# Kernel optimization log

Measured on AMD Instinct MI355X. Metric: run time of the kernel, lower is better.

## Reference

```python
import jax, jax.numpy as jnp
import numpy as np
from jax import lax

B, CIN, T = 16, 2, 4096
DM, DI, DS, DR, DC, NL = 128, 256, 16, 8, 4, 6  # d_model, d_inner, d_state, dt_rank, d_conv, n_layers


def setup_inputs():
    ks = iter(jax.random.split(jax.random.key(0), 48))
    def rn(shape, s=0.05):
        return jax.random.normal(next(ks), shape, jnp.float32) * s
    rng = np.random.default_rng(0)
    n_mask = int(round(0.25 / 0.02))
    starts = rng.choice(np.linspace(0.0, 1.0, int(round(1 / 0.02)), endpoint=False), n_mask, replace=False)
    m = np.ones((B, CIN, T), np.float32)
    for s0 in starts:
        m[:, :, int(T * s0):int(T * (s0 + 0.02))] = 0.0
    return {
        'x': jax.random.normal(next(ks), (B, CIN, T), jnp.float32),
        'mask': jnp.asarray(m),
        'enc_W0': rn((32, CIN, 3), 0.3), 'enc_b0': jnp.zeros(32), 'enc_g0': jnp.ones(32), 'enc_be0': jnp.zeros(32),
        'enc_W1': rn((64, 32, 3), 0.1), 'enc_b1': jnp.zeros(64), 'enc_g1': jnp.ones(64), 'enc_be1': jnp.zeros(64),
        'enc_W2': rn((128, 64, 3), 0.08), 'enc_b2': jnp.zeros(128), 'enc_g2': jnp.ones(128), 'enc_be2': jnp.zeros(128),
        'ln_g': jnp.ones((NL, DM)), 'ln_b': jnp.zeros((NL, DM)),
        'in_W': rn((NL, 2 * DI, DM)), 'conv_W': rn((NL, DI, DC), 0.3), 'conv_b': jnp.zeros((NL, DI)),
        'xp_W': rn((NL, DR + 2 * DS, DI)), 'dt_W': rn((NL, DI, DR), 0.2),
        'dt_b': jnp.full((NL, DI), -4.6, jnp.float32),  # softplus -> dt ~ 0.01
        'A_log': jnp.tile(jnp.log(jnp.arange(1, DS + 1, dtype=jnp.float32)), (NL, DI, 1)),
        'D_p': jnp.ones((NL, DI)), 'out_W': rn((NL, DM, DI)),
        'nf_g': jnp.ones(DM), 'nf_b': jnp.zeros(DM),
        'dec_W0': rn((128, 64, 3), 0.08), 'dec_b0': jnp.zeros(64), 'dec_g0': jnp.ones(64), 'dec_be0': jnp.zeros(64),
        'dec_W1': rn((64, 32, 3), 0.1), 'dec_b1': jnp.zeros(32), 'dec_g1': jnp.ones(32), 'dec_be1': jnp.zeros(32),
        'dec_W2': rn((32, CIN, 3), 0.1), 'dec_b2': jnp.zeros(CIN),
    }


def _conv(x, W, b, stride, pad):
    y = lax.conv_general_dilated(x, W, (stride,), [(pad, pad)], dimension_numbers=('NCH', 'OIH', 'NCH'))
    return y + b[None, :, None]


def _deconv(x, W, b, stride=2, pad=1, out_pad=1):
    # torch ConvTranspose1d weight (in, out, k) -> flipped conv with lhs dilation
    k = W.shape[-1]
    Wc = jnp.flip(W, -1).transpose(1, 0, 2)
    y = lax.conv_general_dilated(x, Wc, (1,), [(k - 1 - pad, k - 1 - pad + out_pad)],
                                 lhs_dilation=(stride,), dimension_numbers=('NCH', 'OIH', 'NCH'))
    return y + b[None, :, None]


def _gn1(x, g, b, eps=1e-5):  # GroupNorm(1, C) over (C, L)
    m = x.mean((1, 2), keepdims=True)
    v = ((x - m) ** 2).mean((1, 2), keepdims=True)
    return (x - m) * lax.rsqrt(v + eps) * g[None, :, None] + b[None, :, None]


def _ln(x, g, b, eps=1e-5):
    m = x.mean(-1, keepdims=True)
    v = ((x - m) ** 2).mean(-1, keepdims=True)
    return (x - m) * lax.rsqrt(v + eps) * g + b


def _mamba(u, in_W, conv_W, conv_b, xp_W, dt_W, dt_b, A_log, D_p, out_W):
    # u: (B, L, DM)
    xz = jnp.einsum('bld,ed->ble', u, in_W)            # (B, L, 2*DI)
    xi, z = xz[..., :DI], xz[..., DI:]
    xc = jnp.pad(xi.transpose(0, 2, 1), ((0, 0), (0, 0), (DC - 1, 0)))  # causal pad
    xc = lax.conv_general_dilated(xc, conv_W[:, None, :], (1,), [(0, 0)],
                                  feature_group_count=DI, dimension_numbers=('NCH', 'OIH', 'NCH'))
    xc = jax.nn.silu(xc + conv_b[None, :, None]).transpose(0, 2, 1)     # (B, L, DI)
    dbl = jnp.einsum('bld,ed->ble', xc, xp_W)          # (B, L, DR+2*DS)
    dt = jax.nn.softplus(jnp.einsum('blr,dr->bld', dbl[..., :DR], dt_W) + dt_b)
    Bm = dbl[..., DR:DR + DS]
    Cm = dbl[..., DR + DS:]
    A = -jnp.exp(A_log)                                # (DI, DS)
    dA = jnp.exp(dt[..., None] * A)                    # (B, L, DI, DS)
    dBx = dt[..., None] * Bm[:, :, None, :] * xc[..., None]
    def comb(e1, e2):
        a1, b1 = e1
        a2, b2 = e2
        return a1 * a2, a2 * b1 + b2
    _, h = lax.associative_scan(comb, (dA, dBx), axis=1)  # selective scan over L
    y = jnp.einsum('blds,bls->bld', h, Cm) + D_p * xc
    y = y * jax.nn.silu(z)
    return jnp.einsum('bld,ed->ble', y, out_W)          # (B, L, DM)


def _forward(x, mask, enc_W0, enc_b0, enc_g0, enc_be0, enc_W1, enc_b1, enc_g1, enc_be1,
             enc_W2, enc_b2, enc_g2, enc_be2, ln_g, ln_b, in_W, conv_W, conv_b, xp_W,
             dt_W, dt_b, A_log, D_p, out_W, nf_g, nf_b,
             dec_W0, dec_b0, dec_g0, dec_be0, dec_W1, dec_b1, dec_g1, dec_be1, dec_W2, dec_b2):
    gelu = lambda t: jax.nn.gelu(t, approximate=False)
    h = mask * x
    h = gelu(_gn1(_conv(h, enc_W0, enc_b0, 2, 1), enc_g0, enc_be0))
    h = gelu(_gn1(_conv(h, enc_W1, enc_b1, 2, 1), enc_g1, enc_be1))
    h = gelu(_gn1(_conv(h, enc_W2, enc_b2, 2, 1), enc_g2, enc_be2))
    s = h.transpose(0, 2, 1)                            # (B, L=T/8, DM)
    for i in range(NL):
        s = s + _mamba(_ln(s, ln_g[i], ln_b[i]), in_W[i], conv_W[i], conv_b[i],
                       xp_W[i], dt_W[i], dt_b[i], A_log[i], D_p[i], out_W[i])
    s = _ln(s, nf_g, nf_b)
    d = s.transpose(0, 2, 1)
    d = gelu(_gn1(_deconv(d, dec_W0, dec_b0), dec_g0, dec_be0))
    d = gelu(_gn1(_deconv(d, dec_W1, dec_b1), dec_g1, dec_be1))
    d = _deconv(d, dec_W2, dec_b2)                      # (B, CIN, T), no norm/act on last block
    return d


def reference(x, mask, enc_W0, enc_b0, enc_g0, enc_be0, enc_W1, enc_b1, enc_g1, enc_be1,
              enc_W2, enc_b2, enc_g2, enc_be2, ln_g, ln_b, in_W, conv_W, conv_b, xp_W,
              dt_W, dt_b, A_log, D_p, out_W, nf_g, nf_b,
              dec_W0, dec_b0, dec_g0, dec_be0, dec_W1, dec_b1, dec_g1, dec_be1, dec_W2, dec_b2):
    d = _forward(x, mask, enc_W0, enc_b0, enc_g0, enc_be0, enc_W1, enc_b1, enc_g1, enc_be1,
                 enc_W2, enc_b2, enc_g2, enc_be2, ln_g, ln_b, in_W, conv_W, conv_b, xp_W,
                 dt_W, dt_b, A_log, D_p, out_W, nf_g, nf_b,
                 dec_W0, dec_b0, dec_g0, dec_be0, dec_W1, dec_b1, dec_g1, dec_be1, dec_W2, dec_b2)
    return (d, x, mask)
```

## Files before the change

kernel.cpp:

```cpp
#include <hip/hip_runtime.h>
#include <hip/hip_bf16.h>
#include <math.h>

#define NB 16
#define TT 4096
#define LL 512
#define DM 128
#define DI 256
#define NLAYER 6
#define CL 32
#define NCH 16

typedef __bf16 bf16x8 __attribute__((ext_vector_type(8)));
typedef float f32x4 __attribute__((ext_vector_type(4)));
typedef unsigned short ushort;

static __device__ __forceinline__ float gelu_f(float v){
  return 0.5f*v*(1.f + erff(v*0.70710678118654752f));
}
static __device__ __forceinline__ float silu_f(float v){
  return v/(1.f + __expf(-v));
}
static __device__ __forceinline__ ushort f2b(float v){
  __hip_bfloat16 h = __float2bfloat16(v);
  return *(ushort*)&h;
}

__global__ __launch_bounds__(256) void k_maskmul(const float* __restrict__ x, const float* __restrict__ m,
                          float* __restrict__ out, int n){
  int i = blockIdx.x*256 + threadIdx.x;
  if (i < n) out[i] = x[i]*m[i];
}

__global__ __launch_bounds__(256) void k_castb(const float* __restrict__ in, ushort* __restrict__ out, int n){
  int i = blockIdx.x*256 + threadIdx.x;
  if (i < n) out[i] = f2b(in[i]);
}

__global__ __launch_bounds__(256) void k_trw(const float* __restrict__ in, float* __restrict__ out, int Ci, int Co){
  int idx = blockIdx.x*256 + threadIdx.x;
  int n = Ci*Co*3;
  if (idx >= n) return;
  int k = idx % 3;
  int o = (idx/3) % Co;
  int ci = idx/(3*Co);
  out[((size_t)o*Ci + ci)*3 + k] = in[idx];
}

template<int Ci, int Co, int TW, int OS>
__global__ __launch_bounds__(256) void k_conv_lds(const float* __restrict__ x, const float* __restrict__ W,
                        const float* __restrict__ bias, float* __restrict__ y, int Li){
  const int Lc = TW;
  const int Lo = Li >> 1;
  const int S  = Lo / Lc;
  const int CoB = Co / OS;
  __shared__ float xe[Ci][Lc+1];
  __shared__ float xo[Ci][Lc+1];
  int bid = blockIdx.x;
  int os = bid % OS;
  int ch = (bid / OS) % S;
  int b  = bid / (OS*S);
  int t0 = ch*Lc;
  const float* xb = x + (size_t)b*Ci*Li;
  for (int idx = threadIdx.x; idx < Ci*(2*Lc+1); idx += 256){
    int ci = idx / (2*Lc+1);
    int j  = idx - ci*(2*Lc+1);
    int gin = 2*t0 - 1 + j;
    float v = (gin >= 0 && gin < Li) ? xb[(size_t)ci*Li + gin] : 0.f;
    if (j & 1) xo[ci][j>>1] = v;
    else       xe[ci][j>>1] = v;
  }
  __syncthreads();
  const int NOg = 256/TW;
  const int OI  = CoB/NOg;
  int tl = threadIdx.x % TW;
  int og = threadIdx.x / TW;
  #pragma unroll
  for (int oi = 0; oi < OI; oi++){
    int o = os*CoB + oi*NOg + og;
    const float* w = W + (size_t)o*Ci*3;
    float acc = bias[o];
    #pragma unroll 4
    for (int ci = 0; ci < Ci; ci++){
      float w0 = w[ci*3+0], w1 = w[ci*3+1], w2 = w[ci*3+2];
      acc += w0*xe[ci][tl] + w1*xo[ci][tl] + w2*xe[ci][tl+1];
    }
    y[((size_t)b*Co + o)*Lo + t0 + tl] = acc;
  }
}

__global__ __launch_bounds__(256) void k_gn_part(const float* __restrict__ x, float* __restrict__ gp){
  int b = blockIdx.x >> 3, k8 = blockIdx.x & 7;
  const float* xb = x + (size_t)b*65536 + (size_t)k8*8192;
  float s = 0.f, s2 = 0.f;
  for (int i = threadIdx.x; i < 8192; i += 256){ float v = xb[i]; s += v; s2 += v*v; }
  #pragma unroll
  for (int o = 32; o; o >>= 1){ s += __shfl_down(s, o); s2 += __shfl_down(s2, o); }
  __shared__ float sh[8];
  int wid = threadIdx.x >> 6;
  if ((threadIdx.x & 63) == 0){ sh[wid] = s; sh[wid+4] = s2; }
  __syncthreads();
  if (threadIdx.x == 0){
    float a = sh[0]+sh[1]+sh[2]+sh[3], a2 = sh[4]+sh[5]+sh[6]+sh[7];
    gp[(b*8+k8)*2+0] = a; gp[(b*8+k8)*2+1] = a2;
  }
}
__global__ __launch_bounds__(256) void k_gn_apply(float* __restrict__ x, const float* __restrict__ g,
                          const float* __restrict__ be, int Tl, const float* __restrict__ gp){
  int gidx = blockIdx.x*256 + threadIdx.x;
  int b = gidx >> 16, i = gidx & 65535;
  float s = 0.f, s2 = 0.f;
  #pragma unroll
  for (int k = 0; k < 8; k++){ s += gp[(b*8+k)*2]; s2 += gp[(b*8+k)*2+1]; }
  float mean = s*(1.f/65536.f);
  float inv  = rsqrtf(s2*(1.f/65536.f) - mean*mean + 1e-5f);
  int c = i / Tl;
  float* p = x + (size_t)b*65536 + i;
  float v = (*p - mean)*inv*g[c] + be[c];
  *p = gelu_f(v);
}

__global__ __launch_bounds__(256) void k_transpose2(const float* __restrict__ in, float* __restrict__ out){
  int idx = blockIdx.x*256 + threadIdx.x;
  if (idx >= NB*DM*LL) return;
  int t = idx & 511;
  int c = (idx >> 9) & 127;
  int b = idx >> 16;
  out[(size_t)b*65536 + (size_t)t*128 + c] = in[idx];
}

__global__ __launch_bounds__(256) void k_transposeB(const float* __restrict__ in, float* __restrict__ out){
  int idx = blockIdx.x*256 + threadIdx.x;
  if (idx >= NB*DM*LL) return;
  int m = idx & 511;
  int c = (idx >> 9) & 127;
  int b = idx >> 16;
  out[idx] = in[(size_t)b*65536 + (size_t)m*128 + c];
}

__global__ __launch_bounds__(256) void k_ln2(const float* __restrict__ x, const float* __restrict__ g,
                      const float* __restrict__ be, float* __restrict__ out, int rows){
  int row = blockIdx.x*4 + (threadIdx.x >> 6);
  if (row >= rows) return;
  int lid = threadIdx.x & 63;
  const float* xr = x + (size_t)row*DM;
  float v0 = xr[lid], v1 = xr[lid+64];
  float s = v0 + v1;
  #pragma unroll
  for (int o = 32; o; o >>= 1) s += __shfl_xor(s, o);
  float mean = s*(1.f/128.f);
  float d0 = v0-mean, d1 = v1-mean;
  float s2 = d0*d0 + d1*d1;
  #pragma unroll
  for (int o = 32; o; o >>= 1) s2 += __shfl_xor(s2, o);
  float inv = rsqrtf(s2*(1.f/128.f) + 1e-5f);
  float* orow = out + (size_t)row*DM;
  orow[lid]    = d0*inv*g[lid]    + be[lid];
  orow[lid+64] = d1*inv*g[lid+64] + be[lid+64];
}

__global__ __launch_bounds__(256) void k_ln2b(const float* __restrict__ x, const float* __restrict__ g,
                      const float* __restrict__ be, ushort* __restrict__ out, int rows){
  int row = blockIdx.x*4 + (threadIdx.x >> 6);
  if (row >= rows) return;
  int lid = threadIdx.x & 63;
  const float* xr = x + (size_t)row*DM;
  float v0 = xr[lid], v1 = xr[lid+64];
  float s = v0 + v1;
  #pragma unroll
  for (int o = 32; o; o >>= 1) s += __shfl_xor(s, o);
  float mean = s*(1.f/128.f);
  float d0 = v0-mean, d1 = v1-mean;
  float s2 = d0*d0 + d1*d1;
  #pragma unroll
  for (int o = 32; o; o >>= 1) s2 += __shfl_xor(s2, o);
  float inv = rsqrtf(s2*(1.f/128.f) + 1e-5f);
  ushort* orow = out + (size_t)row*DM;
  orow[lid]    = f2b(d0*inv*g[lid]    + be[lid]);
  orow[lid+64] = f2b(d1*inv*g[lid+64] + be[lid+64]);
}

__global__ __launch_bounds__(256) void k_mfma_split(const ushort* __restrict__ A, const ushort* __restrict__ B,
                          float* __restrict__ C0, float* __restrict__ C1, int K){
  int tid = threadIdx.x;
  int wid = tid >> 6, l = tid & 63;
  int wm = wid >> 1, wn = wid & 1;
  int m0 = blockIdx.y*128 + wm*64;
  int n0 = blockIdx.x*128 + wn*64;
  int lr = l & 15;
  int lk = (l >> 4)*8;
  int orow = (l >> 4)*4;
  f32x4 acc[4][4];
  #pragma unroll
  for (int i = 0; i < 4; i++)
    #pragma unroll
    for (int j = 0; j < 4; j++) acc[i][j] = (f32x4){0.f,0.f,0.f,0.f};
  for (int k0 = 0; k0 < K; k0 += 32){
    bf16x8 a[4], b[4];
    #pragma unroll
    for (int f = 0; f < 4; f++)
      a[f] = *(const bf16x8*)(A + (size_t)(m0 + f*16 + lr)*K + k0 + lk);
    #pragma unroll
    for (int f = 0; f < 4; f++)
      b[f] = *(const bf16x8*)(B + (size_t)(n0 + f*16 + lr)*K + k0 + lk);
    #pragma unroll
    for (int i = 0; i < 4; i++)
      #pragma unroll
      for (int j = 0; j < 4; j++)
        acc[i][j] = __builtin_amdgcn_mfma_f32_16x16x32_bf16(a[i], b[j], acc[i][j], 0, 0, 0);
  }
  float* C    = (n0 < 256) ? C0 : C1;
  int ncol0   = (n0 < 256) ? n0 : n0 - 256;
  #pragma unroll
  for (int i = 0; i < 4; i++)
    #pragma unroll
    for (int j = 0; j < 4; j++)
      #pragma unroll
      for (int r = 0; r < 4; r++)
        C[(size_t)(m0 + i*16 + orow + r)*256 + ncol0 + j*16 + lr] = acc[i][j][r];
}

__global__ __launch_bounds__(256) void k_mfma_acc(const ushort* __restrict__ A, const ushort* __restrict__ B,
                          float* __restrict__ C, int N, int K){
  int tid = threadIdx.x;
  int wid = tid >> 6, l = tid & 63;
  int wm = wid >> 1, wn = wid & 1;
  int m0 = blockIdx.y*128 + wm*64;
  int n0 = blockIdx.x*128 + wn*64;
  int lr = l & 15;
  int lk = (l >> 4)*8;
  int orow = (l >> 4)*4;
  f32x4 acc[4][4];
  #pragma unroll
  for (int i = 0; i < 4; i++)
    #pragma unroll
    for (int j = 0; j < 4; j++)
      #pragma unroll
      for (int r = 0; r < 4; r++)
        acc[i][j][r] = C[(size_t)(m0 + i*16 + orow + r)*N + n0 + j*16 + lr];
  for (int k0 = 0; k0 < K; k0 += 32){
    bf16x8 a[4], b[4];
    #pragma unroll
    for (int f = 0; f < 4; f++)
      a[f] = *(const bf16x8*)(A + (size_t)(m0 + f*16 + lr)*K + k0 + lk);
    #pragma unroll
    for (int f = 0; f < 4; f++)
      b[f] = *(const bf16x8*)(B + (size_t)(n0 + f*16 + lr)*K + k0 + lk);
    #pragma unroll
    for (int i = 0; i < 4; i++)
      #pragma unroll
      for (int j = 0; j < 4; j++)
        acc[i][j] = __builtin_amdgcn_mfma_f32_16x16x32_bf16(a[i], b[j], acc[i][j], 0, 0, 0);
  }
  #pragma unroll
  for (int i = 0; i < 4; i++)
    #pragma unroll
    for (int j = 0; j < 4; j++)
      #pragma unroll
      for (int r = 0; r < 4; r++)
        C[(size_t)(m0 + i*16 + orow + r)*N + n0 + j*16 + lr] = acc[i][j][r];
}

__global__ __launch_bounds__(256) void k_gemm_xp(const float* __restrict__ A, const float* __restrict__ B,
                          float* __restrict__ C){
  __shared__ float As[32][17];
  __shared__ float Bs[64][17];
  int tid = threadIdx.x;
  int m0 = blockIdx.x*32;
  int tx = tid & 15, ty = tid >> 4;
  float acc[2][4] = {};
  for (int k0 = 0; k0 < 256; k0 += 16){
    if (tid < 128){
      int r = tid >> 2, c = (tid & 3)*4;
      float4 av = *(const float4*)(A + (size_t)(m0+r)*256 + k0 + c);
      As[r][c]=av.x; As[r][c+1]=av.y; As[r][c+2]=av.z; As[r][c+3]=av.w;
    }
    {
      int r = tid >> 2, c = (tid & 3)*4;
      float4 bv = make_float4(0.f,0.f,0.f,0.f);
      if (r < 40) bv = *(const float4*)(B + (size_t)r*256 + k0 + c);
      Bs[r][c]=bv.x; Bs[r][c+1]=bv.y; Bs[r][c+2]=bv.z; Bs[r][c+3]=bv.w;
    }
    __syncthreads();
    #pragma unroll
    for (int k = 0; k < 16; k++){
      float a[2], bb[4];
      #pragma unroll
      for (int i = 0; i < 2; i++) a[i] = As[ty*2+i][k];
      #pragma unroll
      for (int j = 0; j < 4; j++) bb[j] = Bs[tx*4+j][k];
      #pragma unroll
      for (int i = 0; i < 2; i++)
        #pragma unroll
        for (int j = 0; j < 4; j++) acc[i][j] += a[i]*bb[j];
    }
    __syncthreads();
  }
  #pragma unroll
  for (int i = 0; i < 2; i++){
    int m = m0 + ty*2 + i;
    #pragma unroll
    for (int j = 0; j < 4; j++){
      int n = tx*4 + j;
      if (n < 40) C[(size_t)m*40 + n] = acc[i][j];
    }
  }
}

__global__ __launch_bounds__(256) void k_cconv2(const float* __restrict__ xi, const float* __restrict__ cw,
                         const float* __restrict__ cb, float* __restrict__ xc){
  int idx = blockIdx.x*256 + threadIdx.x;
  if (idx >= NB*LL*DI) return;
  int d = idx & 255;
  int l = (idx >> 8) & 511;
  int b = idx >> 17;
  const float* xp = xi + (size_t)b*131072 + d;
  float acc = cb[d];
  #pragma unroll
  for (int j = 0; j < 4; j++){
    int m = l - 3 + j;
    if (m >= 0) acc += xp[(size_t)m*256]*cw[d*4 + j];
  }
  xc[idx] = silu_f(acc);
}

__global__ __launch_bounds__(256) void k_scan_sum(const float* __restrict__ xc, const float* __restrict__ dbl,
                        const float* __restrict__ dtW, const float* __restrict__ dtb,
                        const float* __restrict__ Alog,
                        float* __restrict__ GA, float* __restrict__ GB){
  __shared__ float srow[CL*40];
  int bid = blockIdx.x;
  int b = bid >> 4, ch = bid & 15;
  int d = threadIdx.x;
  const float* dbp = dbl + (size_t)b*20480 + ch*CL*40;
  for (int j = d; j < CL*40; j += 256) srow[j] = dbp[j];
  float4 w0 = *(const float4*)(dtW + d*8);
  float4 w1 = *(const float4*)(dtW + d*8 + 4);
  float tb = dtb[d];
  float a[16];
  #pragma unroll
  for (int s = 0; s < 16; s++) a[s] = -__expf(Alog[d*16 + s]);
  const float* xcp = xc + (size_t)b*131072 + (size_t)ch*CL*256 + d;
  __syncthreads();
  float A[16], Bv[16];
  #pragma unroll
  for (int s = 0; s < 16; s++){ A[s] = 1.f; Bv[s] = 0.f; }
  #pragma unroll 2
  for (int i = 0; i < CL; i++){
    const float* r = srow + i*40;
    float raw = tb + r[0]*w0.x + r[1]*w0.y + r[2]*w0.z + r[3]*w0.w
                   + r[4]*w1.x + r[5]*w1.y + r[6]*w1.z + r[7]*w1.w;
    float dt = (raw > 20.f) ? raw : log1pf(__expf(raw));
    float xcv = xcp[(size_t)i*256];
    float dxc = dt*xcv;
    #pragma unroll
    for (int s = 0; s < 16; s++){
      float e = __expf(dt*a[s]);
      A[s] *= e;
      Bv[s] = e*Bv[s] + dxc*r[8+s];
    }
  }
  size_t base = (((size_t)b*NCH + ch)*16)*256 + d;
  #pragma unroll
  for (int s = 0; s < 16; s++){
    GA[base + (size_t)s*256] = A[s];
    GB[base + (size_t)s*256] = Bv[s];
  }
}

__global__ __launch_bounds__(256) void k_scan_pre(const float* __restrict__ GA, float* __restrict__ GB){
  int gid = blockIdx.x*256 + threadIdx.x;
  int b = gid >> 12;
  int s = (gid >> 8) & 15;
  int d = gid & 255;
  size_t stride = (size_t)16*256;
  size_t idx = (((size_t)b*NCH)*16 + s)*256 + d;
  float P = 0.f;
  #pragma unroll
  for (int ch = 0; ch < NCH; ch++){
    float Ac = GA[idx], Bc = GB[idx];
    GB[idx] = P;
    P = Ac*P + Bc;
    idx += stride;
  }
}

__global__ __launch_bounds__(256) void k_scan_emit(const float* __restrict__ xc, const float* __restrict__ dbl,
                        const float* __restrict__ z,
                        const float* __restrict__ dtW, const float* __restrict__ dtb,
                        const float* __restrict__ Alog, const float* __restrict__ Dp,
                        const float* __restrict__ GB, ushort* __restrict__ yb){
  __shared__ float srow[CL*40];
  int bid = blockIdx.x;
  int b = bid >> 4, ch = bid & 15;
  int d = threadIdx.x;
  const float* dbp = dbl + (size_t)b*20480 + ch*CL*40;
  for (int j = d; j < CL*40; j += 256) srow[j] = dbp[j];
  float4 w0 = *(const float4*)(dtW + d*8);
  float4 w1 = *(const float4*)(dtW + d*8 + 4);
  float tb = dtb[d];
  float Dd = Dp[d];
  float a[16];
  #pragma unroll
  for (int s = 0; s < 16; s++) a[s] = -__expf(Alog[d*16 + s]);
  float h[16];
  size_t base = (((size_t)b*NCH + ch)*16)*256 + d;
  #pragma unroll
  for (int s = 0; s < 16; s++) h[s] = GB[base + (size_t)s*256];
  const float* xcp = xc + (size_t)b*131072 + (size_t)ch*CL*256 + d;
  const float* zp  = z  + (size_t)b*131072 + (size_t)ch*CL*256 + d;
  ushort* yp = yb + (size_t)b*131072 + (size_t)ch*CL*256 + d;
  __syncthreads();
  #pragma unroll 2
  for (int i = 0; i < CL; i++){
    const float* r = srow + i*40;
    float raw = tb + r[0]*w0.x + r[1]*w0.y + r[2]*w0.z + r[3]*w0.w
                   + r[4]*w1.x + r[5]*w1.y + r[6]*w1.z + r[7]*w1.w;
    float dt = (raw > 20.f) ? raw : log1pf(__expf(raw));
    float xcv = xcp[(size_t)i*256];
    float dxc = dt*xcv;
    float y = Dd*xcv;
    #pragma unroll
    for (int s = 0; s < 16; s++){
      float e = __expf(dt*a[s]);
      h[s] = e*h[s] + dxc*r[8+s];
      y += h[s]*r[24+s];
    }
    float zv = zp[(size_t)i*256];
    yp[(size_t)i*256] = f2b(y*silu_f(zv));
  }
}

template<int Ci, int Co, int TW, int OS>
__global__ __launch_bounds__(256) void k_deconv_lds(const float* __restrict__ x, const float* __restrict__ WT,
                          const float* __restrict__ bias, float* __restrict__ y, int Li, int cs){
  const int Lc = TW;
  const int S  = Li / Lc;
  const int CoB = Co / OS;
  __shared__ float xin[Ci][Lc+1];
  int bid = blockIdx.x;
  int os = bid % OS;
  int ch = (bid / OS) % S;
  int b  = bid / (OS*S);
  int m0 = ch*Lc;
  const float* xb = x + (size_t)b*Ci*Li;
  for (int idx = threadIdx.x; idx < Ci*(Lc+1); idx += 256){
    int ci = idx / (Lc+1);
    int q  = idx - ci*(Lc+1);
    int m  = m0 + q;
    xin[ci][q] = (m < Li) ? xb[(size_t)ci*cs + m] : 0.f;
  }
  __syncthreads();
  const int NOg = 256/TW;
  const int OI  = CoB/NOg;
  int tl = threadIdx.x % TW;
  int og = threadIdx.x / TW;
  float* yo = y + (size_t)b*Co*(size_t)(2*Li);
  #pragma unroll
  for (int oi = 0; oi < OI; oi++){
    int o = os*CoB + oi*NOg + og;
    const float* w = WT + (size_t)o*Ci*3;
    float bo = bias[o];
    float even = bo, odd = bo;
    #pragma unroll 4
    for (int ci = 0; ci < Ci; ci++){
      float w0 = w[ci*3+0], w1 = w[ci*3+1], w2 = w[ci*3+2];
      float xm  = xin[ci][tl];
      float xm1 = xin[ci][tl+1];
      even += w1*xm;
      odd  += w2*xm + w0*xm1;
    }
    *(float2*)(yo + (size_t)o*(2*Li) + 2*(m0 + tl)) = make_float2(even, odd);
  }
}

__global__ __launch_bounds__(256) void k_deconv2p(const float* __restrict__ x, const float* __restrict__ W,
                          const float* __restrict__ bias, float* __restrict__ y,
                          int Ci, int Co, int Li, int cs, int S){
  __shared__ float w[384];
  int bid = blockIdx.x;
  int ch = bid % S;
  int o  = (bid / S) % Co;
  int b  = bid / (S*Co);
  for (int j = threadIdx.x; j < Ci*3; j += 256){
    int i = j/3, k = j - 3*i;
    w[j] = W[((size_t)i*Co + o)*3 + k];
  }
  __syncthreads();
  int Lc = Li / S;
  int m0 = ch*Lc;
  const float* xb = x + (size_t)b*Ci*Li;
  float bo = bias[o];
  float* yo = y + ((size_t)b*Co + o)*(size_t)(2*Li);
  for (int idx = threadIdx.x; idx < Lc; idx += 256){
    int m = m0 + idx;
    float even = bo, odd = bo;
    bool has1 = (m + 1 < Li);
    for (int i = 0; i < Ci; i++){
      const float* xr = xb + (size_t)i*cs;
      float xm  = xr[m];
      float xm1 = has1 ? xr[m+1] : 0.f;
      even += w[i*3+1]*xm;
      odd  += w[i*3+2]*xm + w[i*3+0]*xm1;
    }
    *(float2*)(yo + 2*m) = make_float2(even, odd);
  }
}

__global__ __launch_bounds__(256) void k_copyf(const float* __restrict__ in, float* __restrict__ out, int n){
  int i = blockIdx.x*256 + threadIdx.x;
  if (i < n) out[i] = in[i];
}

extern "C" void kernel_launch(void* const* d_in, const int* in_sizes, int n_in,
                              void* d_out, int out_size, void* d_ws, size_t ws_size,
                              hipStream_t stream) {
  const float* x      = (const float*)d_in[0];
  const float* mask   = (const float*)d_in[1];
  const float* enc_W0 = (const float*)d_in[2];
  const float* enc_b0 = (const float*)d_in[3];
  const float* enc_g0 = (const float*)d_in[4];
  const float* enc_be0= (const float*)d_in[5];
  const float* enc_W1 = (const float*)d_in[6];
  const float* enc_b1 = (const float*)d_in[7];
  const float* enc_g1 = (const float*)d_in[8];
  const float* enc_be1= (const float*)d_in[9];
  const float* enc_W2 = (const float*)d_in[10];
  const float* enc_b2 = (const float*)d_in[11];
  const float* enc_g2 = (const float*)d_in[12];
  const float* enc_be2= (const float*)d_in[13];
  const float* ln_g   = (const float*)d_in[14];
  const float* ln_b   = (const float*)d_in[15];
  const float* in_W   = (const float*)d_in[16];
  const float* conv_W = (const float*)d_in[17];
  const float* conv_b = (const float*)d_in[18];
  const float* xp_W   = (const float*)d_in[19];
  const float* dt_W   = (const float*)d_in[20];
  const float* dt_b   = (const float*)d_in[21];
  const float* A_log  = (const float*)d_in[22];
  const float* D_p    = (const float*)d_in[23];
  const float* out_W  = (const float*)d_in[24];
  const float* nf_g   = (const float*)d_in[25];
  const float* nf_b   = (const float*)d_in[26];
  const float* dec_W0 = (const float*)d_in[27];
  const float* dec_b0 = (const float*)d_in[28];
  const float* dec_g0 = (const float*)d_in[29];
  const float* dec_be0= (const float*)d_in[30];
  const float* dec_W1 = (const float*)d_in[31];
  const float* dec_b1 = (const float*)d_in[32];
  const float* dec_g1 = (const float*)d_in[33];
  const float* dec_be1= (const float*)d_in[34];
  const float* dec_W2 = (const float*)d_in[35];
  const float* dec_b2 = (const float*)d_in[36];

  float* out = (float*)d_out;

  float* ws  = (float*)d_ws;
  float* S    = ws;
  float* U    = S    + 1048576;
  float* XI   = U    + 1048576;
  float* Z    = XI   + 2097152;
  float* CBUF = Z    + 2097152;
  float* GA   = CBUF + 2097152;
  float* GB   = GA   + 1048576;
  float* DBL  = GB   + 1048576;
  float* WBIN = DBL  + 327680;
  float* WBOUT= WBIN + 196608;
  float* WT0  = WBOUT+ 98304;
  float* WT1  = WT0  + 24576;
  float* EB0 = XI;
  float* EB1 = XI + 1048576;
  float* H0  = CBUF;
  float* UT  = CBUF;
  float* GNP = DBL;
  ushort* Ub    = (ushort*)U;
  ushort* Yb    = (ushort*)GA;
  ushort* WbIn  = (ushort*)WBIN;
  ushort* WbOut = (ushort*)WBOUT;

  k_castb<<<1536, 256, 0, stream>>>(in_W,  WbIn,  NLAYER*512*DM);
  k_castb<<<768, 256, 0, stream>>>(out_W, WbOut, NLAYER*DM*DI);
  k_trw<<<96, 256, 0, stream>>>(dec_W0, WT0, 128, 64);
  k_trw<<<24, 256, 0, stream>>>(dec_W1, WT1, 64, 32);

  k_maskmul<<<512, 256, 0, stream>>>(x, mask, H0, NB*2*TT);
  k_conv_lds<2,32,64,1><<<512, 256, 0, stream>>>(H0, enc_W0, enc_b0, EB0, 4096);
  k_gn_part<<<128, 256, 0, stream>>>(EB0, GNP);
  k_gn_apply<<<4096, 256, 0, stream>>>(EB0, enc_g0, enc_be0, 2048, GNP);
  k_conv_lds<32,64,32,2><<<1024, 256, 0, stream>>>(EB0, enc_W1, enc_b1, EB1, 2048);
  k_gn_part<<<128, 256, 0, stream>>>(EB1, GNP);
  k_gn_apply<<<4096, 256, 0, stream>>>(EB1, enc_g1, enc_be1, 1024, GNP);
  k_conv_lds<64,128,32,4><<<1024, 256, 0, stream>>>(EB1, enc_W2, enc_b2, EB0, 1024);
  k_gn_part<<<128, 256, 0, stream>>>(EB0, GNP);
  k_gn_apply<<<4096, 256, 0, stream>>>(EB0, enc_g2, enc_be2, 512, GNP);
  k_transpose2<<<4096, 256, 0, stream>>>(EB0, S);

  const int rows = NB*LL;
  for (int i = 0; i < NLAYER; i++){
    k_ln2b<<<2048, 256, 0, stream>>>(S, ln_g + i*DM, ln_b + i*DM, Ub, rows);
    k_mfma_split<<<dim3(4, 64), 256, 0, stream>>>(Ub, WbIn + (size_t)i*512*DM, XI, Z, DM);
    k_cconv2<<<8192, 256, 0, stream>>>(XI, conv_W + (size_t)i*DI*4, conv_b + (size_t)i*DI, CBUF);
    k_gemm_xp<<<256, 256, 0, stream>>>(CBUF, xp_W + (size_t)i*40*DI, DBL);
    k_scan_sum<<<256, 256, 0, stream>>>(CBUF, DBL,
                                        dt_W + (size_t)i*DI*8, dt_b + (size_t)i*DI,
                                        A_log + (size_t)i*DI*16, GA, GB);
    k_scan_pre<<<256, 256, 0, stream>>>(GA, GB);
    k_scan_emit<<<256, 256, 0, stream>>>(CBUF, DBL, Z,
                                         dt_W + (size_t)i*DI*8, dt_b + (size_t)i*DI,
                                         A_log + (size_t)i*DI*16, D_p + (size_t)i*DI, GB, Yb);
    k_mfma_acc<<<dim3(1, 64), 256, 0, stream>>>(Yb, WbOut + (size_t)i*DM*DI, S, DM, DI);
  }

  k_ln2<<<2048, 256, 0, stream>>>(S, nf_g, nf_b, U, rows);
  k_transposeB<<<4096, 256, 0, stream>>>(U, UT);
  k_deconv_lds<128,64,16,2><<<1024, 256, 0, stream>>>(UT, WT0, dec_b0, EB0, 512, 512);
  k_gn_part<<<128, 256, 0, stream>>>(EB0, GNP);
  k_gn_apply<<<4096, 256, 0, stream>>>(EB0, dec_g0, dec_be0, 1024, GNP);
  k_deconv_lds<64,32,32,2><<<1024, 256, 0, stream>>>(EB0, WT1, dec_b1, EB1, 1024, 1024);
  k_gn_part<<<128, 256, 0, stream>>>(EB1, GNP);
  k_gn_apply<<<4096, 256, 0, stream>>>(EB1, dec_g1, dec_be1, 2048, GNP);
  k_deconv2p<<<16*2*8, 256, 0, stream>>>(EB1, dec_W2, dec_b2, out, 32, 2, 2048, 2048, 8);

  k_copyf<<<512, 256, 0, stream>>>(x,    out + 131072, 131072);
  k_copyf<<<512, 256, 0, stream>>>(mask, out + 262144, 131072);
}
```

Baseline: 827.0 us.

## Fuse causal conv with x_proj GEMM and retile out-projection MFMA for more blocks

Merges the depthwise causal conv + SiLU kernel with the x_proj GEMM into one kernel. Each block stages a 16-row time chunk (plus 3 halo rows) in LDS, writes the conv output, and computes the 40-column dbl projection from shared memory. This removes one launch and the re-read of the conv output from global memory. The out-projection accumulate GEMM moves from 64 blocks with 128x128 tiles to 256 blocks with 32x128 tiles, giving more parallelism across CUs at the cost of less reuse per block. The new x_proj dot product runs as scalar FMA from LDS, with each thread reading weights straight from global memory.

Measured after the change: 863.3 us. 1.04x slower.

```diff
diff --git a/kernel.cpp b/kernel.cpp
--- a/kernel.cpp
+++ b/kernel.cpp
@@ -220,108 +220,86 @@
         C[(size_t)(m0 + i*16 + orow + r)*256 + ncol0 + j*16 + lr] = acc[i][j][r];
 }
 
-__global__ __launch_bounds__(256) void k_mfma_acc(const ushort* __restrict__ A, const ushort* __restrict__ B,
-                          float* __restrict__ C, int N, int K){
+__global__ __launch_bounds__(256) void k_mfma_acc2(const ushort* __restrict__ A, const ushort* __restrict__ B,
+                          float* __restrict__ C, int K){
   int tid = threadIdx.x;
   int wid = tid >> 6, l = tid & 63;
-  int wm = wid >> 1, wn = wid & 1;
-  int m0 = blockIdx.y*128 + wm*64;
-  int n0 = blockIdx.x*128 + wn*64;
+  int m0 = blockIdx.x*32;
+  int n0 = wid*32;
   int lr = l & 15;
   int lk = (l >> 4)*8;
   int orow = (l >> 4)*4;
-  f32x4 acc[4][4];
-  #pragma unroll
-  for (int i = 0; i < 4; i++)
-    #pragma unroll
-    for (int j = 0; j < 4; j++)
+  f32x4 acc[2][2];
+  #pragma unroll
+  for (int i = 0; i < 2; i++)
+    #pragma unroll
+    for (int j = 0; j < 2; j++)
       #pragma unroll
       for (int r = 0; r < 4; r++)
-        acc[i][j][r] = C[(size_t)(m0 + i*16 + orow + r)*N + n0 + j*16 + lr];
+        acc[i][j][r] = C[(size_t)(m0 + i*16 + orow + r)*128 + n0 + j*16 + lr];
   for (int k0 = 0; k0 < K; k0 += 32){
-    bf16x8 a[4], b[4];
-    #pragma unroll
-    for (int f = 0; f < 4; f++)
+    bf16x8 a[2], b[2];
+    #pragma unroll
+    for (int f = 0; f < 2; f++)
       a[f] = *(const bf16x8*)(A + (size_t)(m0 + f*16 + lr)*K + k0 + lk);
     #pragma unroll
-    for (int f = 0; f < 4; f++)
+    for (int f = 0; f < 2; f++)
       b[f] = *(const bf16x8*)(B + (size_t)(n0 + f*16 + lr)*K + k0 + lk);
     #pragma unroll
-    for (int i = 0; i < 4; i++)
+    for (int i = 0; i < 2; i++)
       #pragma unroll
-      for (int j = 0; j < 4; j++)
+      for (int j = 0; j < 2; j++)
         acc[i][j] = __builtin_amdgcn_mfma_f32_16x16x32_bf16(a[i], b[j], acc[i][j], 0, 0, 0);
   }
   #pragma unroll
-  for (int i = 0; i < 4; i++)
-    #pragma unroll
-    for (int j = 0; j < 4; j++)
+  for (int i = 0; i < 2; i++)
+    #pragma unroll
+    for (int j = 0; j < 2; j++)
       #pragma unroll
       for (int r = 0; r < 4; r++)
-        C[(size_t)(m0 + i*16 + orow + r)*N + n0 + j*16 + lr] = acc[i][j][r];
-}
-
-__global__ __launch_bounds__(256) void k_gemm_xp(const float* __restrict__ A, const float* __restrict__ B,
-                          float* __restrict__ C){
-  __shared__ float As[32][17];
-  __shared__ float Bs[64][17];
-  int tid = threadIdx.x;
-  int m0 = blockIdx.x*32;
-  int tx = tid & 15, ty = tid >> 4;
-  float acc[2][4] = {};
-  for (int k0 = 0; k0 < 256; k0 += 16){
-    if (tid < 128){
-      int r = tid >> 2, c = (tid & 3)*4;
-      float4 av = *(const float4*)(A + (size_t)(m0+r)*256 + k0 + c);
-      As[r][c]=av.x; As[r][c+1]=av.y; As[r][c+2]=av.z; As[r][c+3]=av.w;
+        C[(size_t)(m0 + i*16 + orow + r)*128 + n0 + j*16 + lr] = acc[i][j][r];
+}
+
+__global__ __launch_bounds__(256) void k_conv_xp(const float* __restrict__ xi, const float* __restrict__ cw,
+                        const float* __restrict__ cb, const float* __restrict__ xpW,
+                        float* __restrict__ xc, float* __restrict__ dbl){
+  __shared__ float xis[19][257];
+  __shared__ float xcs[16][260];
+  int bid = blockIdx.x;
+  int b = bid >> 5, ch = bid & 31;
+  int l0 = ch*16;
+  const float* xb = xi + (size_t)b*131072;
+  int d = threadIdx.x;
+  #pragma unroll
+  for (int r = 0; r < 19; r++){
+    int l = l0 - 3 + r;
+    xis[r][d] = (l >= 0) ? xb[(size_t)l*256 + d] : 0.f;
+  }
+  float4 w4 = *(const float4*)(cw + d*4);
+  float cb0 = cb[d];
+  float* xcg = xc + (size_t)b*131072 + (size_t)l0*256 + d;
+  #pragma unroll
+  for (int r = 0; r < 16; r++){
+    float acc = cb0 + xis[r][d]*w4.x + xis[r+1][d]*w4.y + xis[r+2][d]*w4.z + xis[r+3][d]*w4.w;
+    float v = silu_f(acc);
+    xcs[r][d] = v;
+    xcg[(size_t)r*256] = v;
+  }
+  __syncthreads();
+  float* dbp = dbl + (size_t)b*20480 + l0*40;
+  for (int t = threadIdx.x; t < 640; t += 256){
+    int r = t / 40, n = t - 40*r;
+    const float* wn = xpW + (size_t)n*256;
+    const float* xr = &xcs[r][0];
+    float acc = 0.f;
+    #pragma unroll 4
+    for (int k = 0; k < 256; k += 4){
+      float4 xv = *(const float4*)(xr + k);
+      float4 wv = *(const float4*)(wn + k);
+      acc += xv.x*wv.x + xv.y*wv.y + xv.z*wv.z + xv.w*wv.w;
     }
-    {
-      int r = tid >> 2, c = (tid & 3)*4;
-      float4 bv = make_float4(0.f,0.f,0.f,0.f);
-      if (r < 40) bv = *(const float4*)(B + (size_t)r*256 + k0 + c);
-      Bs[r][c]=bv.x; Bs[r][c+1]=bv.y; Bs[r][c+2]=bv.z; Bs[r][c+3]=bv.w;
-    }
-    __syncthreads();
-    #pragma unroll
-    for (int k = 0; k < 16; k++){
-      float a[2], bb[4];
-      #pragma unroll
-      for (int i = 0; i < 2; i++) a[i] = As[ty*2+i][k];
-      #pragma unroll
-      for (int j = 0; j < 4; j++) bb[j] = Bs[tx*4+j][k];
-      #pragma unroll
-      for (int i = 0; i < 2; i++)
-        #pragma unroll
-        for (int j = 0; j < 4; j++) acc[i][j] += a[i]*bb[j];
-    }
-    __syncthreads();
-  }
-  #pragma unroll
-  for (int i = 0; i < 2; i++){
-    int m = m0 + ty*2 + i;
-    #pragma unroll
-    for (int j = 0; j < 4; j++){
-      int n = tx*4 + j;
-      if (n < 40) C[(size_t)m*40 + n] = acc[i][j];
-    }
-  }
-}
-
-__global__ __launch_bounds__(256) void k_cconv2(const float* __restrict__ xi, const float* __restrict__ cw,
-                         const float* __restrict__ cb, float* __restrict__ xc){
-  int idx = blockIdx.x*256 + threadIdx.x;
-  if (idx >= NB*LL*DI) return;
-  int d = idx & 255;
-  int l = (idx >> 8) & 511;
-  int b = idx >> 17;
-  const float* xp = xi + (size_t)b*131072 + d;
-  float acc = cb[d];
-  #pragma unroll
-  for (int j = 0; j < 4; j++){
-    int m = l - 3 + j;
-    if (m >= 0) acc += xp[(size_t)m*256]*cw[d*4 + j];
-  }
-  xc[idx] = silu_f(acc);
+    dbp[r*40 + n] = acc;
+  }
 }
 
 __global__ __launch_bounds__(256) void k_scan_sum(const float* __restrict__ xc, const float* __restrict__ dbl,
@@ -599,8 +577,8 @@
   for (int i = 0; i < NLAYER; i++){
     k_ln2b<<<2048, 256, 0, stream>>>(S, ln_g + i*DM, ln_b + i*DM, Ub, rows);
     k_mfma_split<<<dim3(4, 64), 256, 0, stream>>>(Ub, WbIn + (size_t)i*512*DM, XI, Z, DM);
-    k_cconv2<<<8192, 256, 0, stream>>>(XI, conv_W + (size_t)i*DI*4, conv_b + (size_t)i*DI, CBUF);
-    k_gemm_xp<<<256, 256, 0, stream>>>(CBUF, xp_W + (size_t)i*40*DI, DBL);
+    k_conv_xp<<<512, 256, 0, stream>>>(XI, conv_W + (size_t)i*DI*4, conv_b + (size_t)i*DI,
+                                       xp_W + (size_t)i*40*DI, CBUF, DBL);
     k_scan_sum<<<256, 256, 0, stream>>>(CBUF, DBL,
                                         dt_W + (size_t)i*DI*8, dt_b + (size_t)i*DI,
                                         A_log + (size_t)i*DI*16, GA, GB);
@@ -608,7 +586,7 @@
     k_scan_emit<<<256, 256, 0, stream>>>(CBUF, DBL, Z,
                                          dt_W + (size_t)i*DI*8, dt_b + (size_t)i*DI,
                                          A_log + (size_t)i*DI*16, D_p + (size_t)i*DI, GB, Yb);
-    k_mfma_acc<<<dim3(1, 64), 256, 0, stream>>>(Yb, WbOut + (size_t)i*DM*DI, S, DM, DI);
+    k_mfma_acc2<<<256, 256, 0, stream>>>(Yb, WbOut + (size_t)i*DM*DI, S, DI);
   }
 
   k_ln2<<<2048, 256, 0, stream>>>(S, nf_g, nf_b, U, rows);
```
